# Performance work log

Hardware: AMD Instinct MI355X
Metric: run time of the kernel (lower is better)

Reference implementation:

```python
import jax, jax.numpy as jnp
import numpy as np

NEG = jnp.float32(-1e9)  # -inf surrogate, safe for logsumexp
EPS = 1e-7               # keras.backend.epsilon()


def _ctc_loss(y_true, y_pred):
    """Faithful K.ctc_batch_cost with full input/label lengths.

    y_true: [B, L] int labels in [0, C-2] (blank = C-1, TF convention)
    y_pred: [B, T, C] softmax probabilities
    returns: [B, 1] negative log-likelihood per sample
    """
    B, T, C = y_pred.shape
    L = y_true.shape[1]
    blank = C - 1
    S = 2 * L + 1  # extended label: blank-interleaved

    logp = jnp.log(y_pred + EPS)  # [B, T, C]

    # Extended label sequence [blank, l1, blank, l2, ..., lL, blank]
    ext = jnp.full((B, S), blank, dtype=jnp.int32).at[:, 1::2].set(
        y_true.astype(jnp.int32))  # [B, S]

    # Skip transition (s-2 -> s) allowed iff ext[s] != blank and ext[s] != ext[s-2]
    skip = jnp.concatenate(
        [jnp.zeros((B, 2), dtype=bool),
         (ext[:, 2:] != blank) & (ext[:, 2:] != ext[:, :-2])],
        axis=1)  # [B, S]

    # Gather lattice log-probs once: [B, T, S]
    lp = jnp.take_along_axis(logp, ext[:, None, :], axis=2)

    # alpha at t=0: only states 0 (blank) and 1 (first label) reachable
    alpha0 = jnp.full((B, S), NEG).at[:, 0].set(lp[:, 0, 0]).at[:, 1].set(lp[:, 0, 1])

    def step(alpha, lp_t):
        a1 = alpha                                                     # stay
        a2 = jnp.pad(alpha[:, :-1], ((0, 0), (1, 0)), constant_values=NEG)  # advance 1
        a3 = jnp.pad(alpha[:, :-2], ((0, 0), (2, 0)), constant_values=NEG)  # advance 2
        a3 = jnp.where(skip, a3, NEG)
        new = lp_t + jax.nn.logsumexp(jnp.stack([a1, a2, a3]), axis=0)
        return new, None

    lp_rest = jnp.transpose(lp[:, 1:, :], (1, 0, 2))  # [T-1, B, S]
    alphaT, _ = jax.lax.scan(step, alpha0, lp_rest)

    # Total log-prob ends in last blank or last label
    ll = jax.nn.logsumexp(alphaT[:, S - 2:S], axis=1)  # [B]
    return -ll[:, None]  # [B, 1], matches ctc_batch_cost's expand_dims


def setup_inputs() -> dict:
    key = jax.random.key(0)
    k1, k2 = jax.random.split(key)
    B, T, C, L = 512, 512, 128, 64
    logits = jax.random.normal(k1, (B, T, C), dtype=jnp.float32)
    y_pred = jax.nn.softmax(logits, axis=-1)  # ctc_batch_cost expects probs
    y_true = jax.random.randint(k2, (B, L), 0, C - 1)  # labels exclude blank C-1
    return {"y_true": y_true, "y_pred": y_pred}


def reference(y_true, y_pred):
    return _ctc_loss(y_true, y_pred)
```

## Files before the change

### kernel.cpp

```cpp
#include <hip/hip_runtime.h>


constexpr float EPSF = 1e-7f;
constexpr float LN2F = 0.6931471805599453f;

template<int CTRL>
__device__ __forceinline__ float dpp_mov(float x) {
    return __int_as_float(__builtin_amdgcn_update_dpp(
        0, __float_as_int(x), CTRL, 0xF, 0xF, true));
}

__global__ __launch_bounds__(64)
void ctc_fwd(const int* __restrict__ y_true,
             const float* __restrict__ y_pred,
             float* __restrict__ out)
{
    const int b    = blockIdx.x;
    const int lane = threadIdx.x;

    const char* __restrict__ base =
        (const char*)(y_pred + (size_t)b * 512 * 128);

    const int   lab   = y_true[b * 64 + lane];
    const int   labp  = __shfl_up(lab, 1, 64);
    const float skipf = (lane > 0 && lab != labp) ? 1.0f : 0.0f;
    const bool  l0    = (lane == 0);

    const int offL = lab * 4;
    const int offB = 127 * 4;

    float pLab[32], pBlank[32];

    #pragma unroll
    for (int r = 0; r < 32; ++r) {
        pLab[r]   = *(const float*)(base + r * 512 + offL);
        pBlank[r] = *(const float*)(base + r * 512 + offB);
    }

    float aZ, aA, aB;
    {
        float pb0 = pBlank[0] + EPSF;
        float pl0 = pLab[0]   + EPSF;
        aZ = pb0;
        aA = l0 ? pl0 : 0.0f;
        aB = 0.0f;
    }

    int   shift = 0;
    float red   = 0.0f;

    auto slot = [&](int t, int u, bool doLoad) {
        float pl = pLab[u]   + EPSF;
        float pb = pBlank[u] + EPSF;
        float upA = dpp_mov<0x138>(aA);
        float upB = dpp_mov<0x138>(aB);
        upB = l0 ? aZ : upB;
        float ts = aA + upB;
        ts = fmaf(skipf, upA, ts);
        float nA = pl * ts;
        float nB = pb * (aB + aA);
        aZ *= pb;
        aA = nA; aB = nB;

        if ((u & 7) == 3) {
            float r = fmaxf(fmaxf(aA, aB), aZ);
            r = fmaxf(r, dpp_mov<0x111>(r));
            r = fmaxf(r, dpp_mov<0x112>(r));
            r = fmaxf(r, dpp_mov<0x114>(r));
            r = fmaxf(r, dpp_mov<0x118>(r));
            r = fmaxf(r, dpp_mov<0x142>(r));
            r = fmaxf(r, dpp_mov<0x143>(r));
            red = r;
        }
        if ((u & 7) == 7) {
            int mb = __builtin_amdgcn_readlane(__float_as_int(red), 63);
            int e  = (mb >> 23) & 0xff;
            int f  = 314 - e;
            f = f < 1 ? 1 : (f > 254 ? 254 : f);
            float scale = __int_as_float(f << 23);
            shift += f - 127;
            aA *= scale; aB *= scale; aZ *= scale;
        }
        if (doLoad) {
            int rn = t + 32; rn = rn > 511 ? 511 : rn;
            pLab[u]   = *(const float*)(base + rn * 512 + offL);
            pBlank[u] = *(const float*)(base + rn * 512 + offB);
        }
    };

    for (int blk = 0; blk < 15; ++blk) {
        int t0 = 1 + blk * 32;
        #pragma unroll
        for (int i = 0; i < 32; ++i)
            slot(t0 + i, (1 + i) & 31, true);
    }
    #pragma unroll
    for (int i = 0; i < 31; ++i)
        slot(481 + i, (482 + i - 1) & 31, false);

    float s   = aA + aB;
    float ll2 = __builtin_amdgcn_logf(s);
    if (lane == 63) out[b] = ((float)shift - ll2) * LN2F;
}

extern "C" void kernel_launch(void* const* d_in, const int* in_sizes, int n_in,
                              void* d_out, int out_size, void* d_ws, size_t ws_size,
                              hipStream_t stream)
{
    const int*   y_true = (const int*)d_in[0];
    const float* y_pred = (const float*)d_in[1];
    float*       out    = (float*)d_out;

    const int B = out_size;
    ctc_fwd<<<dim3(B), dim3(64), 0, stream>>>(y_true, y_pred, out);
}
```

Baseline: 191.4 us.

## Stream y_pred chunks into double-buffered LDS via async global_load_lds

Replaces per-thread register-ring global gathers of label and blank probabilities with bulk coalesced 16-byte global-to-LDS async loads of 64-timestep chunks, double-buffered so the next chunk loads while the current one is processed. Blank probabilities are read once per chunk into one register per lane and broadcast with readlane, while label probabilities come from LDS through a small ring. This targets the scattered, latency-bound 4-byte global loads. In exchange it reads all 128 classes per row instead of about 2, and uses 64KB of LDS per block, which limits occupancy. Synchronization relies on a manual vmcnt wait with no barrier, which is enough only because the block is a single wave.

```diff
diff --git a/kernel.cpp b/kernel.cpp
--- a/kernel.cpp
+++ b/kernel.cpp
@@ -1,4 +1,5 @@
 #include <hip/hip_runtime.h>
+#include <stdint.h>
 
 
 constexpr float EPSF = 1e-7f;
@@ -10,15 +11,23 @@
         0, __float_as_int(x), CTRL, 0xF, 0xF, true));
 }
 
+__device__ __forceinline__ void gload_lds16(const void* g, void* l) {
+    __builtin_amdgcn_global_load_lds(
+        (const __attribute__((address_space(1))) void*)g,
+        (__attribute__((address_space(3))) void*)l, 16, 0, 0);
+}
+
 __global__ __launch_bounds__(64)
 void ctc_fwd(const int* __restrict__ y_true,
              const float* __restrict__ y_pred,
              float* __restrict__ out)
 {
+    __shared__ float lds[2][64][128];
+
     const int b    = blockIdx.x;
     const int lane = threadIdx.x;
 
-    const char* __restrict__ base =
+    const char* __restrict__ gbase =
         (const char*)(y_pred + (size_t)b * 512 * 128);
 
     const int   lab   = y_true[b * 64 + lane];
@@ -26,77 +35,84 @@
     const float skipf = (lane > 0 && lab != labp) ? 1.0f : 0.0f;
     const bool  l0    = (lane == 0);
 
-    const int offL = lab * 4;
-    const int offB = 127 * 4;
-
-    float pLab[32], pBlank[32];
-
-    #pragma unroll
-    for (int r = 0; r < 32; ++r) {
-        pLab[r]   = *(const float*)(base + r * 512 + offL);
-        pBlank[r] = *(const float*)(base + r * 512 + offB);
+    {
+        const char* g = gbase + lane * 16;
+        #pragma unroll
+        for (int j = 0; j < 32; ++j)
+            gload_lds16(g + j * 1024, (char*)&lds[0][0][0] + j * 1024);
     }
 
-    float aZ, aA, aB;
-    {
-        float pb0 = pBlank[0] + EPSF;
-        float pl0 = pLab[0]   + EPSF;
-        aZ = pb0;
-        aA = l0 ? pl0 : 0.0f;
-        aB = 0.0f;
-    }
-
+    float aZ = 0.0f, aA = 0.0f, aB = 0.0f;
     int   shift = 0;
     float red   = 0.0f;
 
-    auto slot = [&](int t, int u, bool doLoad) {
-        float pl = pLab[u]   + EPSF;
-        float pb = pBlank[u] + EPSF;
-        float upA = dpp_mov<0x138>(aA);
-        float upB = dpp_mov<0x138>(aB);
-        upB = l0 ? aZ : upB;
-        float ts = aA + upB;
-        ts = fmaf(skipf, upA, ts);
-        float nA = pl * ts;
-        float nB = pb * (aB + aA);
-        aZ *= pb;
-        aA = nA; aB = nB;
+    #pragma unroll 1
+    for (int c = 0; c < 8; ++c) {
+        if (c < 7) {
+            const char* g = gbase + (size_t)(c + 1) * 32768 + lane * 16;
+            char*       l = (char*)&lds[(c + 1) & 1][0][0];
+            #pragma unroll
+            for (int j = 0; j < 32; ++j)
+                gload_lds16(g + j * 1024, l + j * 1024);
+            asm volatile("s_waitcnt vmcnt(32)" ::: "memory");
+        } else {
+            asm volatile("s_waitcnt vmcnt(0)" ::: "memory");
+        }
 
-        if ((u & 7) == 3) {
-            float r = fmaxf(fmaxf(aA, aB), aZ);
-            r = fmaxf(r, dpp_mov<0x111>(r));
-            r = fmaxf(r, dpp_mov<0x112>(r));
-            r = fmaxf(r, dpp_mov<0x114>(r));
-            r = fmaxf(r, dpp_mov<0x118>(r));
-            r = fmaxf(r, dpp_mov<0x142>(r));
-            r = fmaxf(r, dpp_mov<0x143>(r));
-            red = r;
+        const float* ch = &lds[c & 1][0][0];
+
+        float vB = ch[lane * 128 + 127] + EPSF;
+
+        float ring[8];
+        #pragma unroll
+        for (int j = 0; j < 8; ++j) ring[j] = ch[j * 128 + lab];
+
+        #pragma unroll
+        for (int u = 0; u < 64; ++u) {
+            float pl = ring[u & 7] + EPSF;
+            float pb = __int_as_float(
+                __builtin_amdgcn_readlane(__float_as_int(vB), u));
+
+            if (c == 0 && u == 0) {
+                aZ = pb;
+                aA = l0 ? pl : 0.0f;
+                aB = 0.0f;
+            } else {
+                float upA = dpp_mov<0x138>(aA);
+                float upB = dpp_mov<0x138>(aB);
+                upB = l0 ? aZ : upB;
+                float ts = aA + upB;
+                ts = fmaf(skipf, upA, ts);
+                float nA = pl * ts;
+                float nB = pb * (aB + aA);
+                aZ *= pb;
+                aA = nA; aB = nB;
+            }
+
+            if ((u & 7) == 3) {
+                float r = fmaxf(fmaxf(aA, aB), aZ);
+                r = fmaxf(r, dpp_mov<0x111>(r));
+                r = fmaxf(r, dpp_mov<0x112>(r));
+                r = fmaxf(r, dpp_mov<0x114>(r));
+                r = fmaxf(r, dpp_mov<0x118>(r));
+                r = fmaxf(r, dpp_mov<0x142>(r));
+                r = fmaxf(r, dpp_mov<0x143>(r));
+                red = r;
+            }
+            if ((u & 7) == 7) {
+                int mb = __builtin_amdgcn_readlane(__float_as_int(red), 63);
+                int e  = (mb >> 23) & 0xff;
+                int f  = 314 - e;
+                f = f < 1 ? 1 : (f > 254 ? 254 : f);
+                float scale = __int_as_float(f << 23);
+                shift += f - 127;
+                aA *= scale; aB *= scale; aZ *= scale;
+            }
+
+            if (u < 56)
+                ring[u & 7] = ch[(u + 8) * 128 + lab];
         }
-        if ((u & 7) == 7) {
-            int mb = __builtin_amdgcn_readlane(__float_as_int(red), 63);
-            int e  = (mb >> 23) & 0xff;
-            int f  = 314 - e;
-            f = f < 1 ? 1 : (f > 254 ? 254 : f);
-            float scale = __int_as_float(f << 23);
-            shift += f - 127;
-            aA *= scale; aB *= scale; aZ *= scale;
-        }
-        if (doLoad) {
-            int rn = t + 32; rn = rn > 511 ? 511 : rn;
-            pLab[u]   = *(const float*)(base + rn * 512 + offL);
-            pBlank[u] = *(const float*)(base + rn * 512 + offB);
-        }
-    };
-
-    for (int blk = 0; blk < 15; ++blk) {
-        int t0 = 1 + blk * 32;
-        #pragma unroll
-        for (int i = 0; i < 32; ++i)
-            slot(t0 + i, (1 + i) & 31, true);
     }
-    #pragma unroll
-    for (int i = 0; i < 31; ++i)
-        slot(481 + i, (482 + i - 1) & 31, false);
 
     float s   = aA + aB;
     float ll2 = __builtin_amdgcn_logf(s);
```

After: 193.5 us. No clear change (+1.1%).
